# Performance work log

Measured on AMD Instinct MI355X. Metric: run time of the kernel, lower is better.

The kernel has to match this reference:

```python
import jax, jax.numpy as jnp
import numpy as np

N_NODES = 100000
N_EDGES = 3200000
D = 128


def setup_inputs() -> dict:
    key = jax.random.key(0)
    k_feat, k_src, k_dst, k_w1, k_w2 = jax.random.split(key, 5)
    feat = jax.random.normal(k_feat, (N_NODES, D), dtype=jnp.float32)
    src = jax.random.randint(k_src, (N_EDGES,), 0, N_NODES, dtype=jnp.int32)
    dst = jax.random.randint(k_dst, (N_EDGES,), 0, N_NODES, dtype=jnp.int32)
    eps = jnp.zeros((1,), dtype=jnp.float32)
    s1 = 1.0 / np.sqrt(D)
    W1 = jax.random.normal(k_w1, (D, D), dtype=jnp.float32) * s1
    b1 = jnp.zeros((D,), dtype=jnp.float32)
    W2 = jax.random.normal(k_w2, (D, D), dtype=jnp.float32) * s1
    b2 = jnp.zeros((D,), dtype=jnp.float32)
    return {"feat": feat, "src": src, "dst": dst, "eps": eps,
            "W1": W1, "b1": b1, "W2": W2, "b2": b2}


def reference(feat, src, dst, eps, W1, b1, W2, b2):
    # message passing: copy source features along edges, sum-reduce at dst
    # neigh[v] = sum_{(u,v) in E} feat[u]
    msgs = feat[src]                                  # [E, D] gather
    neigh = jax.ops.segment_sum(msgs, dst, num_segments=feat.shape[0])  # [N, D]
    # GIN update: (1 + eps) * h_v + aggregated neighbors, then MLP
    h = (1.0 + eps[0]) * feat + neigh                 # [N, D]
    h = jax.nn.relu(h @ W1 + b1)                      # [N, D]
    out = h @ W2 + b2                                 # [N, D]
    return out
```

## Files before the change

### kernel.cpp

```cpp
#include <hip/hip_runtime.h>
#include <stdint.h>

#define N_NODES 100000
#define N_EDGES 3200000
#define DIM 128
#define NPAD 100032
#define NBINS 391
#define BCAP 10240
#define EPB 4096
#define PASSU32 3200000
#define WSTR 140

typedef short short8 __attribute__((ext_vector_type(8)));
typedef float f32x4 __attribute__((ext_vector_type(4)));
typedef float f32x2 __attribute__((ext_vector_type(2)));

__device__ __forceinline__ short f2bf(float x) {
    uint32_t u = __builtin_bit_cast(uint32_t, x);
    u += 0x7fffu + ((u >> 16) & 1u);
    return (short)(u >> 16);
}
__device__ __forceinline__ float bflo(uint32_t p) {
    return __builtin_bit_cast(float, p << 16);
}
__device__ __forceinline__ float bfhi(uint32_t p) {
    return __builtin_bit_cast(float, p & 0xffff0000u);
}
__device__ __forceinline__ uint32_t pack2(float x, float y) {
    return (uint32_t)(uint16_t)f2bf(x) | ((uint32_t)(uint16_t)f2bf(y) << 16);
}
__device__ __forceinline__ f32x2 up2(uint32_t p) {
    return (f32x2){ bflo(p), bfhi(p) };
}

__global__ __launch_bounds__(256) void prep_kernel(const float* __restrict__ feat,
                                                   uint32_t* __restrict__ featp,
                                                   const float* __restrict__ w1,
                                                   const float* __restrict__ w2,
                                                   short* __restrict__ w1t,
                                                   short* __restrict__ w2t,
                                                   int* __restrict__ bincnt) {
    int b = blockIdx.x, t = threadIdx.x;
    if (b < 12500) {
        int i = b * 256 + t;
        float4 f = ((const float4*)feat)[i];
        int node = i >> 5;
        int qi = i & 31;
        int p = qi >> 4;
        int ld = qi & 15;
        uint32_t* o = &featp[p * PASSU32 + node * 32 + ld * 2];
        o[0] = pack2(f.x, f.y);
        o[1] = pack2(f.z, f.w);
    } else if (b < 12564) {
        int i = (b - 12500) * 256 + t;
        int k = i >> 7, n = i & 127;
        w1t[n * DIM + k] = f2bf(w1[i]);
        w2t[n * DIM + k] = f2bf(w2[i]);
    } else {
        int i = (b - 12564) * 256 + t;
        bincnt[i] = 0;
    }
}

__global__ __launch_bounds__(256) void bin_kernel(const int* __restrict__ src,
                                                  const int* __restrict__ dst,
                                                  int* __restrict__ bincnt,
                                                  uint32_t* __restrict__ binpair) {
    __shared__ int hist[512];
    __shared__ int scanv[512];
    __shared__ int scan256[256];
    __shared__ int gbase[NBINS];
    __shared__ int cursor[NBINS];
    __shared__ uint32_t sorted[EPB];
    __shared__ int saddr[EPB];
    int t = threadIdx.x;
    for (int i = t; i < 512; i += 256) hist[i] = 0;
    __syncthreads();
    int e0 = blockIdx.x * EPB;
    int nn = min(EPB, N_EDGES - e0);
    int d[16];
#pragma unroll
    for (int i = 0; i < 16; i++) {
        int idx = i * 256 + t;
        d[i] = (idx < nn) ? dst[e0 + idx] : -1;
        if (d[i] >= 0) atomicAdd(&hist[d[i] >> 8], 1);
    }
    __syncthreads();
    int h0 = hist[2 * t], h1 = hist[2 * t + 1];
    scan256[t] = h0 + h1;
    __syncthreads();
    for (int dd = 1; dd < 256; dd <<= 1) {
        int v = (t >= dd) ? scan256[t - dd] : 0;
        __syncthreads();
        scan256[t] += v;
        __syncthreads();
    }
    int pairExcl = scan256[t] - (h0 + h1);
    scanv[2 * t] = pairExcl;
    scanv[2 * t + 1] = pairExcl + h0;
    for (int b = t; b < NBINS; b += 256) {
        int h = hist[b];
        gbase[b] = h ? atomicAdd(&bincnt[b], h) : 0;
        cursor[b] = 0;
    }
    __syncthreads();
#pragma unroll
    for (int i = 0; i < 16; i++) {
        if (d[i] >= 0) {
            int b = d[i] >> 8;
            int slot = atomicAdd(&cursor[b], 1);
            int p = scanv[b] + slot;
            int g = gbase[b] + slot;
            int e = e0 + i * 256 + t;
            sorted[p] = (uint32_t)src[e] | ((uint32_t)(d[i] & 255) << 24);
            saddr[p] = (g < BCAP) ? (b * BCAP + g) : -1;
        }
    }
    __syncthreads();
    for (int i = t; i < nn; i += 256) {
        int a = saddr[i];
        if (a >= 0) binpair[a] = sorted[i];
    }
}

__global__ __launch_bounds__(1024) void csr_kernel(const int* __restrict__ bincnt,
                                                   const uint32_t* __restrict__ binpair,
                                                   int* __restrict__ rowptr,
                                                   int* __restrict__ csr) {
    __shared__ int hist[256];
    __shared__ int cursor[256];
    __shared__ int sc[256];
    __shared__ int red[256];
    __shared__ int binbase_s;
    __shared__ int sorted_s[BCAP];
    int b = blockIdx.x;
    int t = threadIdx.x;
    if (t < 256) {
        int partial = 0;
        for (int j = t; j < b; j += 256) partial += min(bincnt[j], BCAP);
        red[t] = partial;
        hist[t] = 0;
    }
    __syncthreads();
    for (int dd = 128; dd > 0; dd >>= 1) {
        if (t < dd) red[t] += red[t + dd];
        __syncthreads();
    }
    if (t == 0) binbase_s = red[0];
    __syncthreads();
    int binbase = binbase_s;
    int cntb = min(bincnt[b], BCAP);
    const uint32_t* pairs = binpair + (size_t)b * BCAP;
    for (int i = t; i < cntb; i += 1024)
        atomicAdd(&hist[pairs[i] >> 24], 1);
    __syncthreads();
    int val = 0;
    if (t < 256) { val = hist[t]; sc[t] = val; }
    __syncthreads();
    for (int dd = 1; dd < 256; dd <<= 1) {
        int addv = (t < 256 && t >= dd) ? sc[t - dd] : 0;
        __syncthreads();
        if (t < 256) sc[t] += addv;
        __syncthreads();
    }
    if (t < 256) {
        int excl = sc[t] - val;
        rowptr[(b << 8) + t] = binbase + excl;
        cursor[t] = excl;
    }
    __syncthreads();
    for (int i = t; i < cntb; i += 1024) {
        uint32_t p = pairs[i];
        int s2 = atomicAdd(&cursor[p >> 24], 1);
        sorted_s[s2] = (int)(p & 0x00FFFFFFu);
    }
    __syncthreads();
    for (int i = t; i < cntb; i += 1024)
        csr[binbase + i] = sorted_s[i];
}

#define LDQ(qv, sl) do { int _i = __shfl(u, (sl)); \
    qv = *(const uint4*)&featp[_i * 32 + col8 * 4]; } while (0)

#define ACC8(q) do { \
    A01 += up2((q).x); A23 += up2((q).y); A45 += up2((q).z); A67 += up2((q).w); } while (0)

__global__ __launch_bounds__(256) void gather_kernel(const uint32_t* __restrict__ featp,
                                                     const int* __restrict__ rowptr,
                                                     const int* __restrict__ csr,
                                                     const float* __restrict__ eps,
                                                     uint32_t* __restrict__ hbf,
                                                     int poff) {
    int wid = blockIdx.x * 4 + (threadIdx.x >> 6);
    int lane = threadIdx.x & 63;
    int eighth = lane >> 3;
    int col8 = lane & 7;
    if (wid >= N_NODES) {
        if (wid < NPAD && lane < 32) hbf[wid * 64 + poff + lane] = 0;
        return;
    }
    float e1 = 1.0f + eps[0];
    uint4 sf = *(const uint4*)&featp[wid * 32 + col8 * 4];
    f32x2 A01 = (f32x2){0.f, 0.f}, A23 = (f32x2){0.f, 0.f};
    f32x2 A45 = (f32x2){0.f, 0.f}, A67 = (f32x2){0.f, 0.f};
    int start = rowptr[wid], end = rowptr[wid + 1];
    for (int base = start; base < end; base += 64) {
        int m = min(64, end - base);
        int u = (lane < m) ? csr[base + lane] : 0;
        int j = 0;
        for (; j + 32 <= m; j += 32) {
            uint4 q0, q1, q2, q3;
            LDQ(q0, j + eighth);
            LDQ(q1, j + 8 + eighth);
            LDQ(q2, j + 16 + eighth);
            LDQ(q3, j + 24 + eighth);
            ACC8(q0); ACC8(q1); ACC8(q2); ACC8(q3);
        }
        int r = m - j;
        if (r > 0) {
            int mm = m - 1;
            if (r > 24) {
                uint4 q0, q1, q2, q3;
                int p3 = j + 24 + eighth;
                LDQ(q0, j + eighth); LDQ(q1, j + 8 + eighth);
                LDQ(q2, j + 16 + eighth); LDQ(q3, min(p3, mm));
                ACC8(q0); ACC8(q1); ACC8(q2);
                if (p3 < m) ACC8(q3);
            } else if (r > 16) {
                uint4 q0, q1, q2;
                int p2 = j + 16 + eighth;
                LDQ(q0, j + eighth); LDQ(q1, j + 8 + eighth);
                LDQ(q2, min(p2, mm));
                ACC8(q0); ACC8(q1);
                if (p2 < m) ACC8(q2);
            } else if (r > 8) {
                uint4 q0, q1;
                int p1 = j + 8 + eighth;
                LDQ(q0, j + eighth); LDQ(q1, min(p1, mm));
                ACC8(q0);
                if (p1 < m) ACC8(q1);
            } else {
                uint4 q0;
                int p0 = j + eighth;
                LDQ(q0, min(p0, mm));
                if (p0 < m) ACC8(q0);
            }
        }
    }
    float a0 = A01.x, a1 = A01.y, a2 = A23.x, a3 = A23.y;
    float a4 = A45.x, a5 = A45.y, a6 = A67.x, a7 = A67.y;
    a0 += __shfl_xor(a0, 8);  a1 += __shfl_xor(a1, 8);
    a2 += __shfl_xor(a2, 8);  a3 += __shfl_xor(a3, 8);
    a4 += __shfl_xor(a4, 8);  a5 += __shfl_xor(a5, 8);
    a6 += __shfl_xor(a6, 8);  a7 += __shfl_xor(a7, 8);
    a0 += __shfl_xor(a0, 16); a1 += __shfl_xor(a1, 16);
    a2 += __shfl_xor(a2, 16); a3 += __shfl_xor(a3, 16);
    a4 += __shfl_xor(a4, 16); a5 += __shfl_xor(a5, 16);
    a6 += __shfl_xor(a6, 16); a7 += __shfl_xor(a7, 16);
    a0 += __shfl_xor(a0, 32); a1 += __shfl_xor(a1, 32);
    a2 += __shfl_xor(a2, 32); a3 += __shfl_xor(a3, 32);
    a4 += __shfl_xor(a4, 32); a5 += __shfl_xor(a5, 32);
    a6 += __shfl_xor(a6, 32); a7 += __shfl_xor(a7, 32);
    if (eighth == 0) {
        a0 += e1 * bflo(sf.x); a1 += e1 * bfhi(sf.x);
        a2 += e1 * bflo(sf.y); a3 += e1 * bfhi(sf.y);
        a4 += e1 * bflo(sf.z); a5 += e1 * bfhi(sf.z);
        a6 += e1 * bflo(sf.w); a7 += e1 * bfhi(sf.w);
        uint4 w;
        w.x = pack2(a0, a1); w.y = pack2(a2, a3);
        w.z = pack2(a4, a5); w.w = pack2(a6, a7);
        *(uint4*)&hbf[wid * 64 + poff + col8 * 4] = w;
    }
}

__global__ __launch_bounds__(512) void mlp_kernel(const short* __restrict__ hbf,
                                                  const short* __restrict__ w1t,
                                                  const short* __restrict__ w2t,
                                                  const float* __restrict__ b1,
                                                  const float* __restrict__ b2,
                                                  float* __restrict__ out) {
    __shared__ __align__(16) short w1s[128 * WSTR];
    __shared__ __align__(16) short w2s[128 * WSTR];
    __shared__ __align__(16) short h1s[8][16 * WSTR];
    const int t = threadIdx.x;
    for (int c = t; c < 2048; c += 512) {
        int row = c >> 4, cp = c & 15;
        *(short8*)&w1s[row * WSTR + cp * 8] = *(const short8*)&w1t[row * DIM + cp * 8];
        *(short8*)&w2s[row * WSTR + cp * 8] = *(const short8*)&w2t[row * DIM + cp * 8];
    }
    const int wave = t >> 6;
    const int lane = t & 63;
    const int l15 = lane & 15;
    const int quad = lane >> 4;
    short* h1w = &h1s[wave][0];

    float b1v[8], b2v[8];
#pragma unroll
    for (int n = 0; n < 8; n++) {
        b1v[n] = b1[n * 16 + l15];
        b2v[n] = b2[n * 16 + l15];
    }
    __syncthreads();

    const int ngroups = NPAD / 16;
    for (int g = blockIdx.x * 8 + wave; g < ngroups; g += gridDim.x * 8) {
        int row0 = g * 16;
        f32x4 acc[8];
#pragma unroll
        for (int n = 0; n < 8; n++) acc[n] = (f32x4){0.f, 0.f, 0.f, 0.f};
#pragma unroll
        for (int kb = 0; kb < DIM; kb += 32) {
            short8 a = *(const short8*)&hbf[(row0 + l15) * DIM + kb + quad * 8];
#pragma unroll
            for (int n = 0; n < 8; n++) {
                short8 b = *(const short8*)&w1s[(n * 16 + l15) * WSTR + kb + quad * 8];
                acc[n] = __builtin_amdgcn_mfma_f32_16x16x32_bf16(a, b, acc[n], 0, 0, 0);
            }
        }
#pragma unroll
        for (int n = 0; n < 8; n++) {
#pragma unroll
            for (int r = 0; r < 4; r++) {
                float v = acc[n][r] + b1v[n];
                v = v > 0.f ? v : 0.f;
                h1w[(quad * 4 + r) * WSTR + n * 16 + l15] = f2bf(v);
            }
        }
        f32x4 acc2[8];
#pragma unroll
        for (int n = 0; n < 8; n++) acc2[n] = (f32x4){0.f, 0.f, 0.f, 0.f};
#pragma unroll
        for (int kb = 0; kb < DIM; kb += 32) {
            short8 a2 = *(const short8*)&h1w[l15 * WSTR + kb + quad * 8];
#pragma unroll
            for (int n = 0; n < 8; n++) {
                short8 b = *(const short8*)&w2s[(n * 16 + l15) * WSTR + kb + quad * 8];
                acc2[n] = __builtin_amdgcn_mfma_f32_16x16x32_bf16(a2, b, acc2[n], 0, 0, 0);
            }
        }
#pragma unroll
        for (int n = 0; n < 8; n++) {
#pragma unroll
            for (int r = 0; r < 4; r++) {
                int row = row0 + quad * 4 + r;
                if (row < N_NODES)
                    out[row * DIM + n * 16 + l15] = acc2[n][r] + b2v[n];
            }
        }
    }
}

extern "C" void kernel_launch(void* const* d_in, const int* in_sizes, int n_in,
                              void* d_out, int out_size, void* d_ws, size_t ws_size,
                              hipStream_t stream) {
    const float* feat = (const float*)d_in[0];
    const int* src    = (const int*)d_in[1];
    const int* dst    = (const int*)d_in[2];
    const float* eps  = (const float*)d_in[3];
    const float* W1   = (const float*)d_in[4];
    const float* b1   = (const float*)d_in[5];
    const float* W2   = (const float*)d_in[6];
    const float* b2   = (const float*)d_in[7];
    float* out = (float*)d_out;

    char* ws = (char*)d_ws;
    int*      bincnt  = (int*)ws;
    int*      rowptr  = (int*)(ws + 2048);
    int*      csr     = (int*)(ws + 403456);
    uint32_t* binpair = (uint32_t*)(ws + 13203456);
    uint32_t* featp   = (uint32_t*)(ws + 29218816);
    uint32_t* hbf     = (uint32_t*)(ws + 54818816);
    short*    w1t     = (short*)(ws + 80427008);
    short*    w2t     = (short*)(ws + 80459776);

    prep_kernel<<<12566, 256, 0, stream>>>(feat, featp, W1, W2, w1t, w2t, bincnt);
    bin_kernel<<<(N_EDGES + EPB - 1) / EPB, 256, 0, stream>>>(src, dst, bincnt, binpair);
    csr_kernel<<<NBINS, 1024, 0, stream>>>(bincnt, binpair, rowptr, csr);
    gather_kernel<<<NPAD / 4, 256, 0, stream>>>(featp, rowptr, csr, eps, hbf, 0);
    gather_kernel<<<NPAD / 4, 256, 0, stream>>>(featp + PASSU32, rowptr, csr, eps, hbf, 32);
    mlp_kernel<<<256, 512, 0, stream>>>((const short*)hbf, w1t, w2t, b1, b2, out);
}
```

Measured before the change: 310.2 us.

## Replace global atomic bin reservation with deterministic histogram and prefix-scan offsets

Per-block bin offsets no longer come from global atomicAdd on bincnt inside bin_kernel. A separate histogram pass counts per-block, per-bin edges, and a scan kernel computes exclusive offsets and bin totals. bin_kernel then reads its precomputed offsets, so global atomic contention goes away and binpair ordering becomes deterministic. The cost is two extra kernel launches and a second full read of dst.

Result: no change. 305.2 us (-1.6%).

```diff
diff --git a/kernel.cpp b/kernel.cpp
--- a/kernel.cpp
+++ b/kernel.cpp
@@ -6,7 +6,8 @@
 #define DIM 128
 #define NPAD 100032
 #define NBINS 391
-#define BCAP 10240
+#define NBLK 782
+#define BCAP 10176
 #define EPB 4096
 #define PASSU32 3200000
 #define WSTR 140
@@ -38,8 +39,7 @@
                                                    const float* __restrict__ w1,
                                                    const float* __restrict__ w2,
                                                    short* __restrict__ w1t,
-                                                   short* __restrict__ w2t,
-                                                   int* __restrict__ bincnt) {
+                                                   short* __restrict__ w2t) {
     int b = blockIdx.x, t = threadIdx.x;
     if (b < 12500) {
         int i = b * 256 + t;
@@ -51,20 +51,49 @@
         uint32_t* o = &featp[p * PASSU32 + node * 32 + ld * 2];
         o[0] = pack2(f.x, f.y);
         o[1] = pack2(f.z, f.w);
-    } else if (b < 12564) {
+    } else {
         int i = (b - 12500) * 256 + t;
         int k = i >> 7, n = i & 127;
         w1t[n * DIM + k] = f2bf(w1[i]);
         w2t[n * DIM + k] = f2bf(w2[i]);
-    } else {
-        int i = (b - 12564) * 256 + t;
-        bincnt[i] = 0;
-    }
+    }
+}
+
+__global__ __launch_bounds__(256) void hist_kernel(const int* __restrict__ dst,
+                                                   int* __restrict__ ghist) {
+    __shared__ int hist[NBINS];
+    int t = threadIdx.x;
+    for (int i = t; i < NBINS; i += 256) hist[i] = 0;
+    __syncthreads();
+    int e0 = blockIdx.x * EPB;
+    int nn = min(EPB, N_EDGES - e0);
+    for (int i = t; i < nn; i += 256) atomicAdd(&hist[dst[e0 + i] >> 8], 1);
+    __syncthreads();
+    for (int b = t; b < NBINS; b += 256)
+        ghist[b * NBLK + blockIdx.x] = hist[b];
+}
+
+__global__ __launch_bounds__(1024) void offset_kernel(const int* __restrict__ ghist,
+                                                      int* __restrict__ goff,
+                                                      int* __restrict__ bincnt) {
+    __shared__ int s[1024];
+    int b = blockIdx.x, t = threadIdx.x;
+    int v = (t < NBLK) ? ghist[b * NBLK + t] : 0;
+    s[t] = v;
+    __syncthreads();
+    for (int d = 1; d < 1024; d <<= 1) {
+        int x = (t >= d) ? s[t - d] : 0;
+        __syncthreads();
+        s[t] += x;
+        __syncthreads();
+    }
+    if (t < NBLK) goff[b * NBLK + t] = s[t] - v;
+    if (t == NBLK - 1) bincnt[b] = s[t];
 }
 
 __global__ __launch_bounds__(256) void bin_kernel(const int* __restrict__ src,
                                                   const int* __restrict__ dst,
-                                                  int* __restrict__ bincnt,
+                                                  const int* __restrict__ goff,
                                                   uint32_t* __restrict__ binpair) {
     __shared__ int hist[512];
     __shared__ int scanv[512];
@@ -99,8 +128,7 @@
     scanv[2 * t] = pairExcl;
     scanv[2 * t + 1] = pairExcl + h0;
     for (int b = t; b < NBINS; b += 256) {
-        int h = hist[b];
-        gbase[b] = h ? atomicAdd(&bincnt[b], h) : 0;
+        gbase[b] = goff[b * NBLK + blockIdx.x];
         cursor[b] = 0;
     }
     __syncthreads();
@@ -368,13 +396,17 @@
     int*      rowptr  = (int*)(ws + 2048);
     int*      csr     = (int*)(ws + 403456);
     uint32_t* binpair = (uint32_t*)(ws + 13203456);
-    uint32_t* featp   = (uint32_t*)(ws + 29218816);
-    uint32_t* hbf     = (uint32_t*)(ws + 54818816);
-    short*    w1t     = (short*)(ws + 80427008);
-    short*    w2t     = (short*)(ws + 80459776);
-
-    prep_kernel<<<12566, 256, 0, stream>>>(feat, featp, W1, W2, w1t, w2t, bincnt);
-    bin_kernel<<<(N_EDGES + EPB - 1) / EPB, 256, 0, stream>>>(src, dst, bincnt, binpair);
+    uint32_t* featp   = (uint32_t*)(ws + 29118720);
+    uint32_t* hbf     = (uint32_t*)(ws + 54718720);
+    short*    w1t     = (short*)(ws + 80326912);
+    short*    w2t     = (short*)(ws + 80359680);
+    int*      ghist   = (int*)(ws + 54718720);
+    int*      goff    = (int*)(ws + 54718720 + 1223168);
+
+    prep_kernel<<<12564, 256, 0, stream>>>(feat, featp, W1, W2, w1t, w2t);
+    hist_kernel<<<NBLK, 256, 0, stream>>>(dst, ghist);
+    offset_kernel<<<NBINS, 1024, 0, stream>>>(ghist, goff, bincnt);
+    bin_kernel<<<NBLK, 256, 0, stream>>>(src, dst, goff, binpair);
     csr_kernel<<<NBINS, 1024, 0, stream>>>(bincnt, binpair, rowptr, csr);
     gather_kernel<<<NPAD / 4, 256, 0, stream>>>(featp, rowptr, csr, eps, hbf, 0);
     gather_kernel<<<NPAD / 4, 256, 0, stream>>>(featp + PASSU32, rowptr, csr, eps, hbf, 32);
```
